# Performance work log

Measured on AMD Instinct MI355X. Metric: run time of the kernel, lower is better.

## Reference

```python
import jax, jax.numpy as jnp
import numpy as np

N_NODES = 50000
N_EDGES = 800000


def graph_conv(h, W, b, src, dst, n_nodes):
    # DGL GraphConv with norm='both':
    #   out = D_in^{-1/2} * A^T * (D_out^{-1/2} * h) @ W + b
    ones = jnp.ones((src.shape[0],), dtype=h.dtype)
    deg_out = jax.ops.segment_sum(ones, src, num_segments=n_nodes)
    deg_in = jax.ops.segment_sum(ones, dst, num_segments=n_nodes)
    norm_src = jnp.clip(deg_out, 1.0) ** -0.5  # [N]
    norm_dst = jnp.clip(deg_in, 1.0) ** -0.5   # [N]
    msg = (h * norm_src[:, None])[src]          # [E, F] gather
    agg = jax.ops.segment_sum(msg, dst, num_segments=n_nodes)  # [N, F] scatter
    return (agg * norm_dst[:, None]) @ W + b


def setup_inputs() -> dict:
    key = jax.random.key(0)
    ks = jax.random.split(key, 5)
    h = jax.random.normal(ks[0], (N_NODES, 64), dtype=jnp.float32)
    src = jax.random.randint(ks[1], (N_EDGES,), 0, N_NODES, dtype=jnp.int32)
    dst = jax.random.randint(ks[2], (N_EDGES,), 0, N_NODES, dtype=jnp.int32)
    W1 = jax.random.normal(ks[3], (64, 128), dtype=jnp.float32) * (1.0 / np.sqrt(64))
    b1 = jnp.zeros((128,), dtype=jnp.float32)
    W2 = jax.random.normal(ks[4], (128, 64), dtype=jnp.float32) * (1.0 / np.sqrt(128))
    b2 = jnp.zeros((64,), dtype=jnp.float32)
    return {"h": h, "src": src, "dst": dst, "W1": W1, "b1": b1, "W2": W2, "b2": b2}


def reference(h, src, dst, W1, b1, W2, b2):
    n = h.shape[0]
    h1 = jax.nn.relu(graph_conv(h, W1, b1, src, dst, n))
    out = graph_conv(h1, W2, b2, src, dst, n)
    return out
```

## Files before the change

### kernel.cpp

```cpp
#include <hip/hip_runtime.h>


#define NBMAX 512
#define CAPLOG 12
#define CAP (1 << CAPLOG)

__device__ inline unsigned short f2bf(float f) {
    unsigned int u = __float_as_uint(f);
    unsigned int r = (u + 0x7FFFu + ((u >> 16) & 1u)) >> 16;
    return (unsigned short)r;
}
__device__ inline float bf2f_lo(unsigned int u) { return __uint_as_float(u << 16); }
__device__ inline float bf2f_hi(unsigned int u) { return __uint_as_float(u & 0xFFFF0000u); }
__device__ inline float bf2f(unsigned short h) {
    return __uint_as_float((unsigned int)h << 16);
}

__global__ __launch_bounds__(256) void place_direct(const int* __restrict__ src,
        const int* __restrict__ dst, int* __restrict__ cnt_s, int* __restrict__ cnt_d,
        unsigned char* __restrict__ ss, unsigned int* __restrict__ sd,
        int n_edges, int nb) {
    __shared__ int hs[NBMAX], hd[NBMAX], bs[NBMAX], bd[NBMAX];
    for (int i = threadIdx.x; i < nb; i += 256) { hs[i] = 0; hd[i] = 0; }
    __syncthreads();
    int chunk = (n_edges + gridDim.x - 1) / gridDim.x;
    int e0 = blockIdx.x * chunk;
    int e1 = e0 + chunk; if (e1 > n_edges) e1 = n_edges;
    for (int e = e0 + (int)threadIdx.x; e < e1; e += 256) {
        atomicAdd(&hs[src[e] >> 7], 1);
        atomicAdd(&hd[dst[e] >> 7], 1);
    }
    __syncthreads();
    for (int i = threadIdx.x; i < nb; i += 256) {
        int v = hs[i]; bs[i] = v ? atomicAdd(&cnt_s[i], v) : 0; hs[i] = 0;
        v = hd[i];     bd[i] = v ? atomicAdd(&cnt_d[i], v) : 0; hd[i] = 0;
    }
    __syncthreads();
    for (int e = e0 + (int)threadIdx.x; e < e1; e += 256) {
        int s = src[e], d = dst[e];
        int sb = s >> 7, db = d >> 7;
        int ps = bs[sb] + atomicAdd(&hs[sb], 1);
        ss[((size_t)sb << CAPLOG) + ps] = (unsigned char)(s & 127);
        int pd = bd[db] + atomicAdd(&hd[db], 1);
        sd[((size_t)db << CAPLOG) + pd] = ((unsigned int)(d & 127) << 25) | (unsigned int)s;
    }
}

__global__ __launch_bounds__(256) void srcdeg_scale(const float* __restrict__ h,
        const unsigned char* __restrict__ ss, const int* __restrict__ cnt_s,
        float* __restrict__ norm_src, unsigned short* __restrict__ xb, int n) {
    __shared__ int cnt[128];
    __shared__ float nrm[128];
    const int b = blockIdx.x;
    if (threadIdx.x < 128) cnt[threadIdx.x] = 0;
    __syncthreads();
    int used = cnt_s[b];
    const unsigned char* p = ss + ((size_t)b << CAPLOG);
    for (int i = threadIdx.x; i < used; i += 256) atomicAdd(&cnt[p[i]], 1);
    __syncthreads();
    if (threadIdx.x < 128) {
        int c = cnt[threadIdx.x]; if (c < 1) c = 1;
        float s = 1.0f / sqrtf((float)c);
        nrm[threadIdx.x] = s;
        int node = (b << 7) + (int)threadIdx.x;
        if (node < n) norm_src[node] = s;
    }
    __syncthreads();
    int base = b << 7;
    for (int t = threadIdx.x; t < 128 * 16; t += 256) {
        int r = t >> 4, c4 = (t & 15) << 2;
        int node = base + r;
        if (node < n) {
            float s = nrm[r];
            float4 v = *(const float4*)(h + (size_t)node * 64 + c4);
            ushort4 o;
            o.x = f2bf(v.x * s); o.y = f2bf(v.y * s);
            o.z = f2bf(v.z * s); o.w = f2bf(v.w * s);
            *(ushort4*)(xb + (size_t)node * 64 + c4) = o;
        }
    }
}

__global__ __launch_bounds__(256) void bucket_sort(const unsigned int* __restrict__ sd,
        const int* __restrict__ cnt_d, int2* __restrict__ node_rng,
        unsigned short* __restrict__ srt, float* __restrict__ norm_dst, int n) {
    __shared__ int cnt[128], cur[128];
    __shared__ int w0tot;
    const int b = blockIdx.x;
    if (threadIdx.x < 128) cnt[threadIdx.x] = 0;
    __syncthreads();
    int used = cnt_d[b];
    const unsigned int* p = sd + ((size_t)b << CAPLOG);
    for (int i = threadIdx.x; i < used; i += 256) atomicAdd(&cnt[p[i] >> 25], 1);
    __syncthreads();
    int lane = threadIdx.x & 63, wid = threadIdx.x >> 6;
    int v = (threadIdx.x < 128) ? cnt[threadIdx.x] : 0;
    int incl = v;
    #pragma unroll
    for (int d = 1; d < 64; d <<= 1) {
        int t = __shfl_up(incl, d, 64);
        if (lane >= d) incl += t;
    }
    if (threadIdx.x == 63) w0tot = incl;
    __syncthreads();
    if (threadIdx.x < 128) {
        int excl = incl - v + (wid == 1 ? w0tot : 0);
        cur[threadIdx.x] = excl;
        int node = (b << 7) + (int)threadIdx.x;
        if (node < n) {
            int base = b << CAPLOG;
            node_rng[node] = make_int2(base + excl, base + excl + v);
            int c = v; if (c < 1) c = 1;
            norm_dst[node] = 1.0f / sqrtf((float)c);
        }
    }
    __syncthreads();
    for (int i = threadIdx.x; i < used; i += 256) {
        unsigned int e = p[i];
        int l = (int)(e >> 25);
        int pos = atomicAdd(&cur[l], 1);
        srt[((size_t)b << CAPLOG) + pos] = (unsigned short)(e & 0xFFFFu);
    }
}

__global__ __launch_bounds__(256) void gather8(const unsigned short* __restrict__ xb,
        const unsigned short* __restrict__ srt, const int2* __restrict__ node_rng,
        const float* __restrict__ nrm, const float* __restrict__ bias,
        float* __restrict__ out, int n_nodes) {
    int node = blockIdx.x * 4 + (threadIdx.x >> 6);
    if (node >= n_nodes) return;
    int lane = threadIdx.x & 63;
    int g  = lane >> 3;
    int c8 = (lane & 7) * 8;
    int2 rng = node_rng[node];
    int a0 = rng.x, a1 = rng.y;
    float acc[8];
    #pragma unroll
    for (int j = 0; j < 8; ++j) acc[j] = 0.f;
    for (int base = a0; base < a1; base += 16) {
        #pragma unroll
        for (int u = 0; u < 2; ++u) {
            int ei = base + u * 8 + g;
            int idx = ei < a1 ? ei : a1 - 1;
            float msk = ei < a1 ? 1.0f : 0.0f;
            int s = srt[idx];
            const uint4 v = *(const uint4*)(xb + (size_t)s * 64 + c8);
            acc[0] = fmaf(bf2f_lo(v.x), msk, acc[0]);
            acc[1] = fmaf(bf2f_hi(v.x), msk, acc[1]);
            acc[2] = fmaf(bf2f_lo(v.y), msk, acc[2]);
            acc[3] = fmaf(bf2f_hi(v.y), msk, acc[3]);
            acc[4] = fmaf(bf2f_lo(v.z), msk, acc[4]);
            acc[5] = fmaf(bf2f_hi(v.z), msk, acc[5]);
            acc[6] = fmaf(bf2f_lo(v.w), msk, acc[6]);
            acc[7] = fmaf(bf2f_hi(v.w), msk, acc[7]);
        }
    }
    #pragma unroll
    for (int off = 8; off < 64; off <<= 1) {
        #pragma unroll
        for (int j = 0; j < 8; ++j) acc[j] += __shfl_xor(acc[j], off, 64);
    }
    if (g == 0) {
        float s = nrm[node];
        float r[8];
        #pragma unroll
        for (int j = 0; j < 8; ++j) r[j] = acc[j] * s;
        if (bias) {
            #pragma unroll
            for (int j = 0; j < 8; ++j) r[j] += bias[c8 + j];
        }
        float* o = out + (size_t)node * 64 + c8;
        *(float4*)(o)     = make_float4(r[0], r[1], r[2], r[3]);
        *(float4*)(o + 4) = make_float4(r[4], r[5], r[6], r[7]);
    }
}

__global__ __launch_bounds__(256) void gemm1(const float* __restrict__ A,
        const float* __restrict__ W1, const float* __restrict__ b1,
        const float* __restrict__ norm, unsigned short* __restrict__ H1b, int n_nodes) {
    __shared__ float Ws[64 * 128];
    __shared__ float As[64 * 68];
    __shared__ float b1s[128];
    const int tid = threadIdx.x;
    for (int idx = tid; idx < 64 * 128; idx += 256) Ws[idx] = W1[idx];
    if (tid < 128) b1s[tid] = b1[tid];

    const int m0 = blockIdx.x * 64;
    const float4* Ag = (const float4*)(A + (size_t)m0 * 64);
    #pragma unroll
    for (int i = 0; i < 4; ++i) {
        int idx = tid + i * 256;
        int m = idx >> 4;
        int k4 = (idx & 15) * 4;
        float4 v = make_float4(0.f, 0.f, 0.f, 0.f);
        if (m0 + m < n_nodes) v = Ag[idx];
        *(float4*)(As + m * 68 + k4) = v;
    }
    __syncthreads();

    const int tx = tid & 15;
    const int ty = tid >> 4;
    float acc[4][8];
    #pragma unroll
    for (int i = 0; i < 4; ++i)
        #pragma unroll
        for (int j = 0; j < 8; ++j) acc[i][j] = 0.0f;

    const float* Ap = As + ty * 4 * 68;
    const float* Wp = Ws + tx * 8;
    for (int k = 0; k < 64; ++k) {
        float a0 = Ap[k];
        float a1 = Ap[68 + k];
        float a2 = Ap[136 + k];
        float a3 = Ap[204 + k];
        float w[8];
        #pragma unroll
        for (int j = 0; j < 8; ++j) w[j] = Wp[k * 128 + j];
        #pragma unroll
        for (int j = 0; j < 8; ++j) {
            acc[0][j] = fmaf(a0, w[j], acc[0][j]);
            acc[1][j] = fmaf(a1, w[j], acc[1][j]);
            acc[2][j] = fmaf(a2, w[j], acc[2][j]);
            acc[3][j] = fmaf(a3, w[j], acc[3][j]);
        }
    }

    #pragma unroll
    for (int i = 0; i < 4; ++i) {
        int node = m0 + ty * 4 + i;
        if (node < n_nodes) {
            float s = norm[node];
            unsigned short r[8];
            #pragma unroll
            for (int j = 0; j < 8; ++j) {
                float v = acc[i][j] + b1s[tx * 8 + j];
                v = v > 0.0f ? v : 0.0f;
                r[j] = f2bf(v * s);
            }
            unsigned short* o = H1b + (size_t)node * 128 + tx * 8;
            *(ushort4*)(o)     = make_ushort4(r[0], r[1], r[2], r[3]);
            *(ushort4*)(o + 4) = make_ushort4(r[4], r[5], r[6], r[7]);
        }
    }
}

__global__ __launch_bounds__(256) void gemm2b(const unsigned short* __restrict__ H1b,
        const float* __restrict__ W2, unsigned short* __restrict__ y2b, int n_nodes) {
    __shared__ float Ws[128 * 64];
    __shared__ float Hs[64 * 132];
    const int tid = threadIdx.x;
    for (int idx = tid; idx < 128 * 64; idx += 256) Ws[idx] = W2[idx];

    const int m0 = blockIdx.x * 64;
    const ushort4* Hg = (const ushort4*)(H1b + (size_t)m0 * 128);
    #pragma unroll
    for (int i = 0; i < 8; ++i) {
        int idx = tid + i * 256;
        int m = idx >> 5;
        int k4 = (idx & 31) * 4;
        float4 v = make_float4(0.f, 0.f, 0.f, 0.f);
        if (m0 + m < n_nodes) {
            ushort4 u = Hg[idx];
            v.x = bf2f(u.x); v.y = bf2f(u.y); v.z = bf2f(u.z); v.w = bf2f(u.w);
        }
        *(float4*)(Hs + m * 132 + k4) = v;
    }
    __syncthreads();

    const int tx = tid & 15;
    const int ty = tid >> 4;
    float acc[4][4];
    #pragma unroll
    for (int i = 0; i < 4; ++i)
        #pragma unroll
        for (int j = 0; j < 4; ++j) acc[i][j] = 0.0f;

    const float* Ap = Hs + ty * 4 * 132;
    for (int k = 0; k < 128; ++k) {
        float a0 = Ap[k];
        float a1 = Ap[132 + k];
        float a2 = Ap[264 + k];
        float a3 = Ap[396 + k];
        const float4 w = *(const float4*)(Ws + k * 64 + tx * 4);
        acc[0][0] = fmaf(a0, w.x, acc[0][0]); acc[0][1] = fmaf(a0, w.y, acc[0][1]);
        acc[0][2] = fmaf(a0, w.z, acc[0][2]); acc[0][3] = fmaf(a0, w.w, acc[0][3]);
        acc[1][0] = fmaf(a1, w.x, acc[1][0]); acc[1][1] = fmaf(a1, w.y, acc[1][1]);
        acc[1][2] = fmaf(a1, w.z, acc[1][2]); acc[1][3] = fmaf(a1, w.w, acc[1][3]);
        acc[2][0] = fmaf(a2, w.x, acc[2][0]); acc[2][1] = fmaf(a2, w.y, acc[2][1]);
        acc[2][2] = fmaf(a2, w.z, acc[2][2]); acc[2][3] = fmaf(a2, w.w, acc[2][3]);
        acc[3][0] = fmaf(a3, w.x, acc[3][0]); acc[3][1] = fmaf(a3, w.y, acc[3][1]);
        acc[3][2] = fmaf(a3, w.z, acc[3][2]); acc[3][3] = fmaf(a3, w.w, acc[3][3]);
    }

    #pragma unroll
    for (int i = 0; i < 4; ++i) {
        int node = m0 + ty * 4 + i;
        if (node < n_nodes) {
            ushort4 o;
            o.x = f2bf(acc[i][0]); o.y = f2bf(acc[i][1]);
            o.z = f2bf(acc[i][2]); o.w = f2bf(acc[i][3]);
            *(ushort4*)(y2b + (size_t)node * 64 + tx * 4) = o;
        }
    }
}

extern "C" void kernel_launch(void* const* d_in, const int* in_sizes, int n_in,
                              void* d_out, int out_size, void* d_ws, size_t ws_size,
                              hipStream_t stream) {
    const float* h   = (const float*)d_in[0];
    const int*   src = (const int*)d_in[1];
    const int*   dst = (const int*)d_in[2];
    const float* W1  = (const float*)d_in[3];
    const float* b1  = (const float*)d_in[4];
    const float* W2  = (const float*)d_in[5];
    const float* b2  = (const float*)d_in[6];
    float* out = (float*)d_out;

    const int n = in_sizes[0] / 64;
    const int E = in_sizes[1];
    const int nb = (n + 127) >> 7;

    char* p = (char*)d_ws;
    auto alloc = [&](size_t bytes) {
        void* r = (void*)p;
        p += (bytes + 255) & ~(size_t)255;
        return r;
    };
    float* agg1          = (float*)alloc((size_t)n * 64 * 4);
    float* norm_src      = (float*)alloc((size_t)n * 4);
    float* norm_dst      = (float*)alloc((size_t)n * 4);
    int2* node_rng       = (int2*)alloc((size_t)n * 8);
    int* cnt2            = (int*)alloc((size_t)2 * nb * 4);
    int* cnt_s = cnt2;
    int* cnt_d = cnt2 + nb;
    unsigned int* sd     = (unsigned int*)alloc((size_t)nb * CAP * 4);
    unsigned short* xb   = (unsigned short*)alloc((size_t)n * 64 * 2);
    unsigned short* H1b  = (unsigned short*)alloc((size_t)n * 128 * 2);
    unsigned short* y2b  = (unsigned short*)alloc((size_t)n * 64 * 2);
    unsigned short* srt  = (unsigned short*)alloc((size_t)nb * CAP * 2);
    unsigned char* ssb   = (unsigned char*)alloc((size_t)nb * CAP);

    hipMemsetAsync(cnt2, 0, 2 * (size_t)nb * sizeof(int), stream);

    place_direct<<<256, 256, 0, stream>>>(src, dst, cnt_s, cnt_d, ssb, sd, E, nb);
    srcdeg_scale<<<nb, 256, 0, stream>>>(h, ssb, cnt_s, norm_src, xb, n);
    bucket_sort<<<nb, 256, 0, stream>>>(sd, cnt_d, node_rng, srt, norm_dst, n);

    int gb = (n + 3) / 4;
    gather8<<<gb, 256, 0, stream>>>(xb, srt, node_rng, norm_dst, nullptr, agg1, n);

    int tb = (n + 63) / 64;
    gemm1<<<tb, 256, 0, stream>>>(agg1, W1, b1, norm_src, H1b, n);
    gemm2b<<<tb, 256, 0, stream>>>(H1b, W2, y2b, n);

    gather8<<<gb, 256, 0, stream>>>(y2b, srt, node_rng, norm_dst, b2, out, n);
}
```

Baseline: 198.7 us.

## Fuse prep kernels, store first aggregate in bf16, unroll gather by three

Merges the source-degree scaling and destination bucket sort into one kernel, cutting a launch. The first gather now writes its aggregate as bf16 instead of fp32, halving that intermediate's write traffic and gemm1's read traffic. The gather loop now handles 24 edges per iteration instead of 16, giving more loads in flight. The bf16 intermediate adds rounding error, and the merged kernel runs its two phases one after the other inside each block.

```diff
diff --git a/kernel.cpp b/kernel.cpp
--- a/kernel.cpp
+++ b/kernel.cpp
@@ -46,67 +46,71 @@
     }
 }
 
-__global__ __launch_bounds__(256) void srcdeg_scale(const float* __restrict__ h,
+__global__ __launch_bounds__(256) void prep(const float* __restrict__ h,
         const unsigned char* __restrict__ ss, const int* __restrict__ cnt_s,
-        float* __restrict__ norm_src, unsigned short* __restrict__ xb, int n) {
-    __shared__ int cnt[128];
+        const unsigned int* __restrict__ sd, const int* __restrict__ cnt_d,
+        float* __restrict__ norm_src, unsigned short* __restrict__ xb,
+        int2* __restrict__ node_rng, unsigned short* __restrict__ srt,
+        float* __restrict__ norm_dst, int n) {
+    __shared__ int cnt[128], cur[128];
     __shared__ float nrm[128];
-    const int b = blockIdx.x;
-    if (threadIdx.x < 128) cnt[threadIdx.x] = 0;
-    __syncthreads();
-    int used = cnt_s[b];
-    const unsigned char* p = ss + ((size_t)b << CAPLOG);
-    for (int i = threadIdx.x; i < used; i += 256) atomicAdd(&cnt[p[i]], 1);
-    __syncthreads();
-    if (threadIdx.x < 128) {
-        int c = cnt[threadIdx.x]; if (c < 1) c = 1;
-        float s = 1.0f / sqrtf((float)c);
-        nrm[threadIdx.x] = s;
-        int node = (b << 7) + (int)threadIdx.x;
-        if (node < n) norm_src[node] = s;
-    }
-    __syncthreads();
-    int base = b << 7;
-    for (int t = threadIdx.x; t < 128 * 16; t += 256) {
-        int r = t >> 4, c4 = (t & 15) << 2;
-        int node = base + r;
-        if (node < n) {
-            float s = nrm[r];
-            float4 v = *(const float4*)(h + (size_t)node * 64 + c4);
-            ushort4 o;
-            o.x = f2bf(v.x * s); o.y = f2bf(v.y * s);
-            o.z = f2bf(v.z * s); o.w = f2bf(v.w * s);
-            *(ushort4*)(xb + (size_t)node * 64 + c4) = o;
-        }
-    }
-}
-
-__global__ __launch_bounds__(256) void bucket_sort(const unsigned int* __restrict__ sd,
-        const int* __restrict__ cnt_d, int2* __restrict__ node_rng,
-        unsigned short* __restrict__ srt, float* __restrict__ norm_dst, int n) {
-    __shared__ int cnt[128], cur[128];
     __shared__ int w0tot;
     const int b = blockIdx.x;
-    if (threadIdx.x < 128) cnt[threadIdx.x] = 0;
+    const int tid = threadIdx.x;
+
+    if (tid < 128) cnt[tid] = 0;
+    __syncthreads();
+    {
+        int used = cnt_s[b];
+        const unsigned char* p = ss + ((size_t)b << CAPLOG);
+        for (int i = tid; i < used; i += 256) atomicAdd(&cnt[p[i]], 1);
+    }
+    __syncthreads();
+    if (tid < 128) {
+        int c = cnt[tid]; if (c < 1) c = 1;
+        float s = 1.0f / sqrtf((float)c);
+        nrm[tid] = s;
+        int node = (b << 7) + tid;
+        if (node < n) norm_src[node] = s;
+    }
+    __syncthreads();
+    {
+        int base = b << 7;
+        for (int t = tid; t < 128 * 16; t += 256) {
+            int r = t >> 4, c4 = (t & 15) << 2;
+            int node = base + r;
+            if (node < n) {
+                float s = nrm[r];
+                float4 v = *(const float4*)(h + (size_t)node * 64 + c4);
+                ushort4 o;
+                o.x = f2bf(v.x * s); o.y = f2bf(v.y * s);
+                o.z = f2bf(v.z * s); o.w = f2bf(v.w * s);
+                *(ushort4*)(xb + (size_t)node * 64 + c4) = o;
+            }
+        }
+    }
+    __syncthreads();
+
+    if (tid < 128) cnt[tid] = 0;
     __syncthreads();
     int used = cnt_d[b];
     const unsigned int* p = sd + ((size_t)b << CAPLOG);
-    for (int i = threadIdx.x; i < used; i += 256) atomicAdd(&cnt[p[i] >> 25], 1);
-    __syncthreads();
-    int lane = threadIdx.x & 63, wid = threadIdx.x >> 6;
-    int v = (threadIdx.x < 128) ? cnt[threadIdx.x] : 0;
+    for (int i = tid; i < used; i += 256) atomicAdd(&cnt[p[i] >> 25], 1);
+    __syncthreads();
+    int lane = tid & 63, wid = tid >> 6;
+    int v = (tid < 128) ? cnt[tid] : 0;
     int incl = v;
     #pragma unroll
     for (int d = 1; d < 64; d <<= 1) {
         int t = __shfl_up(incl, d, 64);
         if (lane >= d) incl += t;
     }
-    if (threadIdx.x == 63) w0tot = incl;
-    __syncthreads();
-    if (threadIdx.x < 128) {
+    if (tid == 63) w0tot = incl;
+    __syncthreads();
+    if (tid < 128) {
         int excl = incl - v + (wid == 1 ? w0tot : 0);
-        cur[threadIdx.x] = excl;
-        int node = (b << 7) + (int)threadIdx.x;
+        cur[tid] = excl;
+        int node = (b << 7) + tid;
         if (node < n) {
             int base = b << CAPLOG;
             node_rng[node] = make_int2(base + excl, base + excl + v);
@@ -115,7 +119,7 @@
         }
     }
     __syncthreads();
-    for (int i = threadIdx.x; i < used; i += 256) {
+    for (int i = tid; i < used; i += 256) {
         unsigned int e = p[i];
         int l = (int)(e >> 25);
         int pos = atomicAdd(&cur[l], 1);
@@ -123,10 +127,10 @@
     }
 }
 
-__global__ __launch_bounds__(256) void gather8(const unsigned short* __restrict__ xb,
+__global__ __launch_bounds__(256) void gather24(const unsigned short* __restrict__ xb,
         const unsigned short* __restrict__ srt, const int2* __restrict__ node_rng,
         const float* __restrict__ nrm, const float* __restrict__ bias,
-        float* __restrict__ out, int n_nodes) {
+        void* __restrict__ outp, int write_bf, int n_nodes) {
     int node = blockIdx.x * 4 + (threadIdx.x >> 6);
     if (node >= n_nodes) return;
     int lane = threadIdx.x & 63;
@@ -137,9 +141,9 @@
     float acc[8];
     #pragma unroll
     for (int j = 0; j < 8; ++j) acc[j] = 0.f;
-    for (int base = a0; base < a1; base += 16) {
-        #pragma unroll
-        for (int u = 0; u < 2; ++u) {
+    for (int base = a0; base < a1; base += 24) {
+        #pragma unroll
+        for (int u = 0; u < 3; ++u) {
             int ei = base + u * 8 + g;
             int idx = ei < a1 ? ei : a1 - 1;
             float msk = ei < a1 ? 1.0f : 0.0f;
@@ -165,17 +169,26 @@
         float r[8];
         #pragma unroll
         for (int j = 0; j < 8; ++j) r[j] = acc[j] * s;
-        if (bias) {
+        if (write_bf) {
+            unsigned short rb[8];
             #pragma unroll
-            for (int j = 0; j < 8; ++j) r[j] += bias[c8 + j];
-        }
-        float* o = out + (size_t)node * 64 + c8;
-        *(float4*)(o)     = make_float4(r[0], r[1], r[2], r[3]);
-        *(float4*)(o + 4) = make_float4(r[4], r[5], r[6], r[7]);
-    }
-}
-
-__global__ __launch_bounds__(256) void gemm1(const float* __restrict__ A,
+            for (int j = 0; j < 8; ++j) rb[j] = f2bf(r[j]);
+            unsigned short* o = (unsigned short*)outp + (size_t)node * 64 + c8;
+            *(ushort4*)(o)     = make_ushort4(rb[0], rb[1], rb[2], rb[3]);
+            *(ushort4*)(o + 4) = make_ushort4(rb[4], rb[5], rb[6], rb[7]);
+        } else {
+            if (bias) {
+                #pragma unroll
+                for (int j = 0; j < 8; ++j) r[j] += bias[c8 + j];
+            }
+            float* o = (float*)outp + (size_t)node * 64 + c8;
+            *(float4*)(o)     = make_float4(r[0], r[1], r[2], r[3]);
+            *(float4*)(o + 4) = make_float4(r[4], r[5], r[6], r[7]);
+        }
+    }
+}
+
+__global__ __launch_bounds__(256) void gemm1(const unsigned short* __restrict__ Ab,
         const float* __restrict__ W1, const float* __restrict__ b1,
         const float* __restrict__ norm, unsigned short* __restrict__ H1b, int n_nodes) {
     __shared__ float Ws[64 * 128];
@@ -186,14 +199,17 @@
     if (tid < 128) b1s[tid] = b1[tid];
 
     const int m0 = blockIdx.x * 64;
-    const float4* Ag = (const float4*)(A + (size_t)m0 * 64);
+    const ushort4* Ag = (const ushort4*)(Ab + (size_t)m0 * 64);
     #pragma unroll
     for (int i = 0; i < 4; ++i) {
         int idx = tid + i * 256;
         int m = idx >> 4;
         int k4 = (idx & 15) * 4;
         float4 v = make_float4(0.f, 0.f, 0.f, 0.f);
-        if (m0 + m < n_nodes) v = Ag[idx];
+        if (m0 + m < n_nodes) {
+            ushort4 u = Ag[idx];
+            v.x = bf2f(u.x); v.y = bf2f(u.y); v.z = bf2f(u.z); v.w = bf2f(u.w);
+        }
         *(float4*)(As + m * 68 + k4) = v;
     }
     __syncthreads();
@@ -326,7 +342,6 @@
         p += (bytes + 255) & ~(size_t)255;
         return r;
     };
-    float* agg1          = (float*)alloc((size_t)n * 64 * 4);
     float* norm_src      = (float*)alloc((size_t)n * 4);
     float* norm_dst      = (float*)alloc((size_t)n * 4);
     int2* node_rng       = (int2*)alloc((size_t)n * 8);
@@ -335,6 +350,7 @@
     int* cnt_d = cnt2 + nb;
     unsigned int* sd     = (unsigned int*)alloc((size_t)nb * CAP * 4);
     unsigned short* xb   = (unsigned short*)alloc((size_t)n * 64 * 2);
+    unsigned short* agg1b= (unsigned short*)alloc((size_t)n * 64 * 2);
     unsigned short* H1b  = (unsigned short*)alloc((size_t)n * 128 * 2);
     unsigned short* y2b  = (unsigned short*)alloc((size_t)n * 64 * 2);
     unsigned short* srt  = (unsigned short*)alloc((size_t)nb * CAP * 2);
@@ -343,15 +359,17 @@
     hipMemsetAsync(cnt2, 0, 2 * (size_t)nb * sizeof(int), stream);
 
     place_direct<<<256, 256, 0, stream>>>(src, dst, cnt_s, cnt_d, ssb, sd, E, nb);
-    srcdeg_scale<<<nb, 256, 0, stream>>>(h, ssb, cnt_s, norm_src, xb, n);
-    bucket_sort<<<nb, 256, 0, stream>>>(sd, cnt_d, node_rng, srt, norm_dst, n);
+    prep<<<nb, 256, 0, stream>>>(h, ssb, cnt_s, sd, cnt_d, norm_src, xb,
+                                 node_rng, srt, norm_dst, n);
 
     int gb = (n + 3) / 4;
-    gather8<<<gb, 256, 0, stream>>>(xb, srt, node_rng, norm_dst, nullptr, agg1, n);
+    gather24<<<gb, 256, 0, stream>>>(xb, srt, node_rng, norm_dst, nullptr,
+                                     (void*)agg1b, 1, n);
 
     int tb = (n + 63) / 64;
-    gemm1<<<tb, 256, 0, stream>>>(agg1, W1, b1, norm_src, H1b, n);
+    gemm1<<<tb, 256, 0, stream>>>(agg1b, W1, b1, norm_src, H1b, n);
     gemm2b<<<tb, 256, 0, stream>>>(H1b, W2, y2b, n);
 
-    gather8<<<gb, 256, 0, stream>>>(y2b, srt, node_rng, norm_dst, b2, out, n);
-}
+    gather24<<<gb, 256, 0, stream>>>(y2b, srt, node_rng, norm_dst, b2,
+                                     (void*)out, 0, n);
+}
```

Measured after the change: 195.8 us. Within noise of the previous version (-1.4%).
